# Performance work log

Hardware: AMD Instinct MI355X
Metric: run time of the kernel (lower is better)

The kernel has to match this reference:

```python
import jax, jax.numpy as jnp
import numpy as np

N = 100000      # nodes
E = 3200000     # edges (avg degree 32)
D = 128         # embed_dim
STEP = 1        # number of gnn_conv steps


def setup_inputs() -> dict:
    key = jax.random.key(0)
    k1, k2, k3, k4, k5 = jax.random.split(key, 5)
    hidden = jax.random.normal(k1, (N, D), dtype=jnp.float32)
    src = jax.random.randint(k2, (E,), 0, N)
    dst = jax.random.randint(k3, (E,), 0, N)
    # nn.Linear(D, 3D, bias=False) -> store transposed as [D, 3D] for h @ W
    W_h = jax.random.normal(k4, (D, 3 * D), dtype=jnp.float32) * 0.05
    W_hf = jax.random.normal(k5, (D, 2 * D), dtype=jnp.float32) * 0.05
    return {"hidden": hidden, "src": src, "dst": dst, "W_h": W_h, "W_hf": W_hf}


def _graph_conv(h, src, dst, n):
    # DGL GraphConv(norm='both', weight=False, bias=False):
    # h_dst = d_in(dst)^{-1/2} * sum_{(src->dst)} d_out(src)^{-1/2} * h_src
    ones = jnp.ones(src.shape[0], dtype=h.dtype)
    out_deg = jnp.clip(jax.ops.segment_sum(ones, src, num_segments=n), 1.0)
    in_deg = jnp.clip(jax.ops.segment_sum(ones, dst, num_segments=n), 1.0)
    h_norm = h * jax.lax.rsqrt(out_deg)[:, None]          # [N, D]
    agg = jax.ops.segment_sum(h_norm[src], dst, num_segments=n)  # [N, D]
    return agg * jax.lax.rsqrt(in_deg)[:, None]


def reference(hidden, src, dst, W_h, W_hf):
    n = hidden.shape[0]
    seqs = []
    for _ in range(STEP):
        h1, h2, h3 = jnp.split(hidden @ W_h, 3, axis=-1)   # each [N, D]
        conv = _graph_conv(h1, src, dst, n)                 # sparse aggregation
        f1, f2 = jnp.split(conv @ W_hf, 2, axis=-1)         # each [N, D]
        gate = jax.nn.relu(f1 + h2)
        hidden = h3 + gate * f2
        seqs.append(hidden)
    return hidden, jnp.stack(seqs, axis=1).mean(axis=1)
```

## Files before the change

kernel.cpp:

```cpp
#include <hip/hip_runtime.h>

#define N_NODES 100000
#define N_EDGES 3200000
#define DIM 128

#define NB 391
#define GCAP 9216
#define PCHUNK 4096

typedef __attribute__((ext_vector_type(8))) short bf16x8;
typedef __attribute__((ext_vector_type(4))) float f32x4;

__device__ __forceinline__ unsigned short f2bf(float x) {
    unsigned u = __float_as_uint(x);
    unsigned r = (u + 0x7FFF + ((u >> 16) & 1)) >> 16;
    return (unsigned short)r;
}

__device__ __forceinline__ void gld_lds16(const unsigned short* src, unsigned short* dst) {
    __builtin_amdgcn_global_load_lds(
        (const __attribute__((address_space(1))) unsigned int*)src,
        (__attribute__((address_space(3))) unsigned int*)dst, 16, 0, 0);
}

__global__ __launch_bounds__(256) void partition_kernel(const int* __restrict__ src,
                                                        const int* __restrict__ dst,
                                                        int* __restrict__ gcnt_d,
                                                        int* __restrict__ gcnt_s,
                                                        unsigned* __restrict__ bstore_d,
                                                        unsigned* __restrict__ bstore_s) {
    __shared__ int hist_d[NB], hofs_d[NB], cur_d[NB];
    __shared__ int hist_s[NB], hofs_s[NB], cur_s[NB];
    int t = threadIdx.x;
    for (int b = t; b < NB; b += 256) {
        hist_d[b] = 0; cur_d[b] = 0;
        hist_s[b] = 0; cur_s[b] = 0;
    }
    __syncthreads();
    int e0 = blockIdx.x * PCHUNK;
    int n = min(PCHUNK, N_EDGES - e0);
    for (int i = t; i < n; i += 256) {
        int s = src[e0 + i];
        int d = dst[e0 + i];
        atomicAdd(&hist_d[d >> 8], 1);
        atomicAdd(&hist_s[s >> 8], 1);
    }
    __syncthreads();
    for (int b = t; b < NB; b += 256) {
        hofs_d[b] = (hist_d[b] > 0) ? atomicAdd(&gcnt_d[b], hist_d[b]) : 0;
        hofs_s[b] = (hist_s[b] > 0) ? atomicAdd(&gcnt_s[b], hist_s[b]) : 0;
    }
    __syncthreads();
    for (int i = t; i < n; i += 256) {
        int s = src[e0 + i];
        int d = dst[e0 + i];
        int bd = d >> 8;
        int pd = hofs_d[bd] + atomicAdd(&cur_d[bd], 1);
        if (pd < GCAP)
            bstore_d[(size_t)bd * GCAP + pd] = ((unsigned)(d & 255) << 24) | (unsigned)s;
        int bs = s >> 8;
        int ps = hofs_s[bs] + atomicAdd(&cur_s[bs], 1);
        if (ps < GCAP)
            bstore_s[(size_t)bs * GCAP + ps] = (unsigned)(s & 255);
    }
}

__global__ void scanb_kernel(const int* __restrict__ gcnt_d, int* __restrict__ bucket_base,
                             int* __restrict__ row_start) {
    __shared__ int v[512];
    int t = threadIdx.x;
    v[t] = (t < NB) ? min(gcnt_d[t], GCAP) : 0;
    __syncthreads();
    for (int off = 1; off < 512; off <<= 1) {
        int x = (t >= off) ? v[t - off] : 0;
        __syncthreads();
        v[t] += x;
        __syncthreads();
    }
    if (t < NB) bucket_base[t + 1] = v[t];
    if (t == 0) {
        bucket_base[0] = 0;
        row_start[N_NODES] = v[NB - 1];
    }
}

__global__ __launch_bounds__(256) void count_kernel(const int* __restrict__ gcnt_s,
                                                    const unsigned* __restrict__ bstore_s,
                                                    float* __restrict__ rn_out) {
    __shared__ int lcnt[256];
    int b = blockIdx.x;
    int t = threadIdx.x;
    lcnt[t] = 0;
    __syncthreads();
    int cnt = min(gcnt_s[b], GCAP);
    const unsigned* bs = &bstore_s[(size_t)b * GCAP];
    for (int i = t; i < cnt; i += 256)
        atomicAdd(&lcnt[bs[i] & 255], 1);
    __syncthreads();
    int node = b * 256 + t;
    if (node < N_NODES)
        rn_out[node] = rsqrtf((float)max(lcnt[t], 1));
}

__global__ __launch_bounds__(256) void fill2_kernel(const int* __restrict__ gcnt_d,
                                                    const unsigned* __restrict__ bstore_d,
                                                    const int* __restrict__ bucket_base,
                                                    int* __restrict__ col,
                                                    int* __restrict__ row_start,
                                                    float* __restrict__ rn_in) {
    __shared__ int lcnt[256];
    __shared__ int lpre[256];
    __shared__ int lcur[256];
    __shared__ int stage[GCAP];
    int b = blockIdx.x;
    int t = threadIdx.x;
    int node0 = b * 256;
    int nn = min(256, N_NODES - node0);
    lcnt[t] = 0;
    __syncthreads();
    int cnt = min(gcnt_d[b], GCAP);
    int base = bucket_base[b];
    const unsigned* bs = &bstore_d[(size_t)b * GCAP];
    for (int i = t; i < cnt; i += 256)
        atomicAdd(&lcnt[bs[i] >> 24], 1);
    __syncthreads();
    int myc = lcnt[t];
    lpre[t] = myc;
    __syncthreads();
    for (int off = 1; off < 256; off <<= 1) {
        int x = (t >= off) ? lpre[t - off] : 0;
        __syncthreads();
        lpre[t] += x;
        __syncthreads();
    }
    int excl = lpre[t] - myc;
    if (t < nn) {
        row_start[node0 + t] = base + excl;
        rn_in[node0 + t] = rsqrtf((float)max(myc, 1));
    }
    lcur[t] = excl;
    __syncthreads();
    for (int i = t; i < cnt; i += 256) {
        unsigned e = bs[i];
        int p = atomicAdd(&lcur[e >> 24], 1);
        stage[p] = (int)(e & 0xFFFFFF);
    }
    __syncthreads();
    for (int i = t; i < cnt; i += 256)
        col[base + i] = stage[i];
}

__global__ void packw_kernel(const float* __restrict__ W_h, const float* __restrict__ W_hf,
                             unsigned short* __restrict__ W1_t,
                             unsigned short* __restrict__ W23_t,
                             unsigned short* __restrict__ Wf_t) {
    int idx = blockIdx.x * 256 + threadIdx.x;
    if (idx < 16384) {
        int n = idx >> 7, k = idx & 127;
        W1_t[idx] = f2bf(W_h[k * 384 + n]);
    } else if (idx < 49152) {
        int j = idx - 16384;
        int n = j >> 7, k = j & 127;
        W23_t[j] = f2bf(W_h[k * 384 + 128 + n]);
    } else if (idx < 81920) {
        int j = idx - 49152;
        int n = j >> 7, k = j & 127;
        Wf_t[j] = f2bf(W_hf[k * 256 + n]);
    }
}

__global__ __launch_bounds__(256) void packh_kernel(const float* __restrict__ hidden,
                                                    unsigned short* __restrict__ hidden_bf) {
    int i = (blockIdx.x * 256 + threadIdx.x) * 8;
    float4 a = *reinterpret_cast<const float4*>(&hidden[i]);
    float4 b = *reinterpret_cast<const float4*>(&hidden[i + 4]);
    ushort4 lo, hi;
    lo.x = f2bf(a.x); lo.y = f2bf(a.y); lo.z = f2bf(a.z); lo.w = f2bf(a.w);
    hi.x = f2bf(b.x); hi.y = f2bf(b.y); hi.z = f2bf(b.z); hi.w = f2bf(b.w);
    *reinterpret_cast<ushort4*>(&hidden_bf[i]) = lo;
    *reinterpret_cast<ushort4*>(&hidden_bf[i + 4]) = hi;
}

__global__ __launch_bounds__(256) void gemm1_mfma(const unsigned short* __restrict__ hidden_bf,
                                                  const unsigned short* __restrict__ W1_t,
                                                  const float* __restrict__ rn_out,
                                                  unsigned short* __restrict__ h1n) {
    __shared__ __align__(16) unsigned short Bs[16384];
    int t = threadIdx.x;
    int row0 = blockIdx.x * 64;
    int lane = t & 63;
    int wave = t >> 6;
    int wr0 = wave * 16;
    int m = lane & 15;
    int q = lane >> 4;

    int arow = min(row0 + wr0 + m, N_NODES - 1);
    bf16x8 af[4];
#pragma unroll
    for (int kc = 0; kc < 4; ++kc)
        af[kc] = *reinterpret_cast<const bf16x8*>(&hidden_bf[arow * 128 + kc * 32 + q * 8]);
    float s4[4];
#pragma unroll
    for (int reg = 0; reg < 4; ++reg) {
        int row = row0 + wr0 + q * 4 + reg;
        s4[reg] = (row < N_NODES) ? rn_out[row] : 0.f;
    }

#pragma unroll
    for (int i = 0; i < 8; ++i) {
        int G = i * 256 + t;
        int row = G >> 4;
        int kseg = G & 15;
        gld_lds16(&W1_t[row * 128 + ((kseg ^ (row & 7)) * 8)], &Bs[G * 8]);
    }
    __syncthreads();

    f32x4 accn[8];
#pragma unroll
    for (int nt = 0; nt < 8; ++nt) {
        f32x4 acc = {0.f, 0.f, 0.f, 0.f};
#pragma unroll
        for (int kc = 0; kc < 4; ++kc) {
            int g = (nt * 16 + m) * 16 + ((kc * 4 + q) ^ (m & 7));
            bf16x8 b = *reinterpret_cast<const bf16x8*>(&Bs[g * 8]);
            acc = __builtin_amdgcn_mfma_f32_16x16x32_bf16(af[kc], b, acc, 0, 0, 0);
        }
        accn[nt] = acc;
    }
    __syncthreads();

    unsigned short (*Sg)[136] = reinterpret_cast<unsigned short (*)[136]>(&Bs[0]);
#pragma unroll
    for (int nt = 0; nt < 8; ++nt)
#pragma unroll
        for (int reg = 0; reg < 4; ++reg)
            Sg[wr0 + q * 4 + reg][nt * 16 + m] = f2bf(accn[nt][reg] * s4[reg]);
    __syncthreads();
    int seg = (t & 15) * 8;
    int rb = t >> 4;
#pragma unroll
    for (int i = 0; i < 4; ++i) {
        int r = rb + i * 16;
        int row = row0 + r;
        if (row < N_NODES)
            *reinterpret_cast<int4*>(&h1n[row * 128 + seg]) =
                *reinterpret_cast<const int4*>(&Sg[r][seg]);
    }
}

__global__ __launch_bounds__(256) void aggregate_kernel(const unsigned* __restrict__ h1n,
                                                        const int* __restrict__ row_start,
                                                        const int* __restrict__ col,
                                                        const float* __restrict__ rn_in,
                                                        unsigned* __restrict__ conv_bf) {
    int wave = threadIdx.x >> 6;
    int lane = threadIdx.x & 63;
    int node = blockIdx.x * 4 + wave;
    if (node >= N_NODES) return;
    int start = row_start[node];
    int end = row_start[node + 1];
    float ax0 = 0.f, ax1 = 0.f, ay0 = 0.f, ay1 = 0.f;
    for (int j = start; j < end; j += 64) {
        int cnt = min(64, end - j);
        int myc = (lane < cnt) ? col[j + lane] : 0;
        int i = 0;
        for (; i + 16 <= cnt; i += 16) {
            unsigned u[16];
#pragma unroll
            for (int k = 0; k < 16; ++k) {
                int s = __builtin_amdgcn_readlane(myc, i + k);
                u[k] = h1n[s * 64 + lane];
            }
#pragma unroll
            for (int k = 0; k < 16; k += 2) {
                ax0 += __uint_as_float(u[k] << 16);
                ay0 += __uint_as_float(u[k] & 0xFFFF0000u);
                ax1 += __uint_as_float(u[k + 1] << 16);
                ay1 += __uint_as_float(u[k + 1] & 0xFFFF0000u);
            }
        }
        for (; i + 4 <= cnt; i += 4) {
            unsigned u[4];
#pragma unroll
            for (int k = 0; k < 4; ++k) {
                int s = __builtin_amdgcn_readlane(myc, i + k);
                u[k] = h1n[s * 64 + lane];
            }
#pragma unroll
            for (int k = 0; k < 4; k += 2) {
                ax0 += __uint_as_float(u[k] << 16);
                ay0 += __uint_as_float(u[k] & 0xFFFF0000u);
                ax1 += __uint_as_float(u[k + 1] << 16);
                ay1 += __uint_as_float(u[k + 1] & 0xFFFF0000u);
            }
        }
        for (; i < cnt; ++i) {
            int s = __builtin_amdgcn_readlane(myc, i);
            unsigned u = h1n[s * 64 + lane];
            ax0 += __uint_as_float(u << 16);
            ay0 += __uint_as_float(u & 0xFFFF0000u);
        }
    }
    float rn = rn_in[node];
    float ax = ax0 + ax1, ay = ay0 + ay1;
    unsigned packed = ((unsigned)f2bf(ay * rn) << 16) | (unsigned)f2bf(ax * rn);
    conv_bf[node * 64 + lane] = packed;
}

__global__ __launch_bounds__(256) void final_mfma(const unsigned short* __restrict__ hidden_bf,
                                                  const unsigned short* __restrict__ conv_bf,
                                                  const unsigned short* __restrict__ W23_t,
                                                  const unsigned short* __restrict__ Wf_t,
                                                  float* __restrict__ out) {
    __shared__ __align__(16) unsigned short Bst[2][8192];
    int t = threadIdx.x;
    int row0 = blockIdx.x * 64;
    int lane = t & 63;
    int wave = t >> 6;
    int wr0 = wave * 16;
    int m = lane & 15;
    int q = lane >> 4;

    int arow = min(row0 + wr0 + m, N_NODES - 1);
    bf16x8 ah[4], ac[4];
#pragma unroll
    for (int kc = 0; kc < 4; ++kc) {
        int o = arow * 128 + kc * 32 + q * 8;
        ah[kc] = *reinterpret_cast<const bf16x8*>(&hidden_bf[o]);
        ac[kc] = *reinterpret_cast<const bf16x8*>(&conv_bf[o]);
    }

    auto stage = [&](int nt, int buf) {
#pragma unroll
        for (int i = 0; i < 4; ++i) {
            int rowin = t >> 4;
            int kseg = t & 15;
            int srow = ((i & 1) ? (nt + 8) : nt) * 16 + rowin;
            const unsigned short* Wp = (i < 2) ? W23_t : Wf_t;
            gld_lds16(&Wp[srow * 128 + ((kseg ^ (rowin & 7)) * 8)],
                      &Bst[buf][(i * 256 + t) * 8]);
        }
    };

    stage(0, 0);
    __syncthreads();

#pragma unroll
    for (int nt = 0; nt < 8; ++nt) {
        if (nt < 7) stage(nt + 1, (nt + 1) & 1);
        const unsigned short* Bb = Bst[nt & 1];
        f32x4 h2 = {0.f, 0.f, 0.f, 0.f}, h3 = {0.f, 0.f, 0.f, 0.f};
        f32x4 f1 = {0.f, 0.f, 0.f, 0.f}, f2 = {0.f, 0.f, 0.f, 0.f};
#pragma unroll
        for (int kc = 0; kc < 4; ++kc) {
            int ks = (kc * 4 + q) ^ (m & 7);
            bf16x8 b2  = *reinterpret_cast<const bf16x8*>(&Bb[(0 * 256 + m * 16 + ks) * 8]);
            bf16x8 b3  = *reinterpret_cast<const bf16x8*>(&Bb[(1 * 256 + m * 16 + ks) * 8]);
            bf16x8 bf1 = *reinterpret_cast<const bf16x8*>(&Bb[(2 * 256 + m * 16 + ks) * 8]);
            bf16x8 bf2 = *reinterpret_cast<const bf16x8*>(&Bb[(3 * 256 + m * 16 + ks) * 8]);
            h2 = __builtin_amdgcn_mfma_f32_16x16x32_bf16(ah[kc], b2, h2, 0, 0, 0);
            h3 = __builtin_amdgcn_mfma_f32_16x16x32_bf16(ah[kc], b3, h3, 0, 0, 0);
            f1 = __builtin_amdgcn_mfma_f32_16x16x32_bf16(ac[kc], bf1, f1, 0, 0, 0);
            f2 = __builtin_amdgcn_mfma_f32_16x16x32_bf16(ac[kc], bf2, f2, 0, 0, 0);
        }
        int colb = nt * 16 + m;
#pragma unroll
        for (int reg = 0; reg < 4; ++reg) {
            int row = row0 + wr0 + q * 4 + reg;
            float g = fmaxf(f1[reg] + h2[reg], 0.f);
            float o = h3[reg] + g * f2[reg];
            if (row < N_NODES) {
                out[(size_t)row * 128 + colb] = o;
                out[(size_t)(N_NODES + row) * 128 + colb] = o;
            }
        }
        __syncthreads();
    }
}

extern "C" void kernel_launch(void* const* d_in, const int* in_sizes, int n_in,
                              void* d_out, int out_size, void* d_ws, size_t ws_size,
                              hipStream_t stream) {
    const float* hidden = (const float*)d_in[0];
    const int* src = (const int*)d_in[1];
    const int* dst = (const int*)d_in[2];
    const float* W_h = (const float*)d_in[3];
    const float* W_hf = (const float*)d_in[4];
    float* out = (float*)d_out;

    auto align_up = [](size_t x) { return (x + 255) & ~(size_t)255; };
    char* p = (char*)d_ws;
    size_t off = 0;
    unsigned short* h1n = (unsigned short*)(p + off); off += align_up((size_t)N_NODES * 128 * 2);
    unsigned short* conv_bf = (unsigned short*)(p + off); off += align_up((size_t)N_NODES * 128 * 2);
    unsigned short* hidden_bf = (unsigned short*)(p + off); off += align_up((size_t)N_NODES * 128 * 2);
    int* col = (int*)(p + off); off += align_up((size_t)N_EDGES * 4);
    unsigned* bstore_d = (unsigned*)(p + off); off += align_up((size_t)NB * GCAP * 4);
    unsigned* bstore_s = (unsigned*)(p + off); off += align_up((size_t)NB * GCAP * 4);
    int* gcnt_d = (int*)(p + off); off += align_up((size_t)NB * 4);
    int* gcnt_s = (int*)(p + off); off += align_up((size_t)NB * 4);
    int* bucket_base = (int*)(p + off); off += align_up((size_t)(NB + 1) * 4);
    int* row_start = (int*)(p + off); off += align_up((size_t)(N_NODES + 1) * 4);
    float* rn_out = (float*)(p + off); off += align_up((size_t)N_NODES * 4);
    float* rn_in = (float*)(p + off); off += align_up((size_t)N_NODES * 4);
    unsigned short* W1_t = (unsigned short*)(p + off); off += align_up((size_t)128 * 128 * 2);
    unsigned short* W23_t = (unsigned short*)(p + off); off += align_up((size_t)256 * 128 * 2);
    unsigned short* Wf_t = (unsigned short*)(p + off); off += align_up((size_t)256 * 128 * 2);

    (void)hipMemsetAsync(gcnt_d, 0, (size_t)NB * 4, stream);
    (void)hipMemsetAsync(gcnt_s, 0, (size_t)NB * 4, stream);

    partition_kernel<<<(N_EDGES + PCHUNK - 1) / PCHUNK, 256, 0, stream>>>(
        src, dst, gcnt_d, gcnt_s, bstore_d, bstore_s);
    scanb_kernel<<<1, 512, 0, stream>>>(gcnt_d, bucket_base, row_start);
    count_kernel<<<NB, 256, 0, stream>>>(gcnt_s, bstore_s, rn_out);
    fill2_kernel<<<NB, 256, 0, stream>>>(gcnt_d, bstore_d, bucket_base, col, row_start, rn_in);
    packw_kernel<<<(81920 + 255) / 256, 256, 0, stream>>>(W_h, W_hf, W1_t, W23_t, Wf_t);
    packh_kernel<<<(N_NODES * 128) / (256 * 8), 256, 0, stream>>>(hidden, hidden_bf);
    gemm1_mfma<<<(N_NODES + 63) / 64, 256, 0, stream>>>(hidden_bf, W1_t, rn_out, h1n);
    aggregate_kernel<<<(N_NODES + 3) / 4, 256, 0, stream>>>(
        (const unsigned*)h1n, row_start, col, rn_in, (unsigned*)conv_bf);
    final_mfma<<<(N_NODES + 63) / 64, 256, 0, stream>>>(hidden_bf, conv_bf, W23_t, Wf_t, out);
}
```

Baseline: 451.8 us.

## Stage partitioned edges in LDS by bucket before writing, shrink src bucket store to bytes

```diff
diff --git a/kernel.cpp b/kernel.cpp
--- a/kernel.cpp
+++ b/kernel.cpp
@@ -28,14 +28,16 @@
                                                         int* __restrict__ gcnt_d,
                                                         int* __restrict__ gcnt_s,
                                                         unsigned* __restrict__ bstore_d,
-                                                        unsigned* __restrict__ bstore_s) {
-    __shared__ int hist_d[NB], hofs_d[NB], cur_d[NB];
-    __shared__ int hist_s[NB], hofs_s[NB], cur_s[NB];
-    int t = threadIdx.x;
-    for (int b = t; b < NB; b += 256) {
-        hist_d[b] = 0; cur_d[b] = 0;
-        hist_s[b] = 0; cur_s[b] = 0;
-    }
+                                                        unsigned char* __restrict__ bstore_s) {
+    __shared__ int hist_d[NB], cur_d[NB], hofs_d[NB];
+    __shared__ int hist_s[NB], cur_s[NB], hofs_s[NB];
+    __shared__ int vsc_d[512], vsc_s[512];
+    __shared__ unsigned stage_d[PCHUNK];
+    __shared__ unsigned short bmap_d[PCHUNK];
+    __shared__ unsigned char stage_s[PCHUNK];
+    __shared__ unsigned short bmap_s[PCHUNK];
+    int t = threadIdx.x;
+    for (int b = t; b < NB; b += 256) { hist_d[b] = 0; hist_s[b] = 0; }
     __syncthreads();
     int e0 = blockIdx.x * PCHUNK;
     int n = min(PCHUNK, N_EDGES - e0);
@@ -50,18 +52,48 @@
         hofs_d[b] = (hist_d[b] > 0) ? atomicAdd(&gcnt_d[b], hist_d[b]) : 0;
         hofs_s[b] = (hist_s[b] > 0) ? atomicAdd(&gcnt_s[b], hist_s[b]) : 0;
     }
+    vsc_d[t]       = (t < NB) ? hist_d[t] : 0;
+    vsc_d[t + 256] = (t + 256 < NB) ? hist_d[t + 256] : 0;
+    vsc_s[t]       = (t < NB) ? hist_s[t] : 0;
+    vsc_s[t + 256] = (t + 256 < NB) ? hist_s[t + 256] : 0;
+    __syncthreads();
+    for (int off = 1; off < 512; off <<= 1) {
+        int d0 = (t >= off) ? vsc_d[t - off] : 0;
+        int d1 = vsc_d[t + 256 - off];
+        int s0 = (t >= off) ? vsc_s[t - off] : 0;
+        int s1 = vsc_s[t + 256 - off];
+        __syncthreads();
+        vsc_d[t] += d0; vsc_d[t + 256] += d1;
+        vsc_s[t] += s0; vsc_s[t + 256] += s1;
+        __syncthreads();
+    }
+    for (int b = t; b < NB; b += 256) {
+        cur_d[b] = b ? vsc_d[b - 1] : 0;
+        cur_s[b] = b ? vsc_s[b - 1] : 0;
+    }
     __syncthreads();
     for (int i = t; i < n; i += 256) {
         int s = src[e0 + i];
         int d = dst[e0 + i];
         int bd = d >> 8;
-        int pd = hofs_d[bd] + atomicAdd(&cur_d[bd], 1);
-        if (pd < GCAP)
-            bstore_d[(size_t)bd * GCAP + pd] = ((unsigned)(d & 255) << 24) | (unsigned)s;
+        int p = atomicAdd(&cur_d[bd], 1);
+        stage_d[p] = ((unsigned)(d & 255) << 24) | (unsigned)s;
+        bmap_d[p] = (unsigned short)bd;
         int bs = s >> 8;
-        int ps = hofs_s[bs] + atomicAdd(&cur_s[bs], 1);
-        if (ps < GCAP)
-            bstore_s[(size_t)bs * GCAP + ps] = (unsigned)(s & 255);
+        int ps = atomicAdd(&cur_s[bs], 1);
+        stage_s[ps] = (unsigned char)(s & 255);
+        bmap_s[ps] = (unsigned short)bs;
+    }
+    __syncthreads();
+    for (int i = t; i < n; i += 256) {
+        int bd = bmap_d[i];
+        int excl = bd ? vsc_d[bd - 1] : 0;
+        int gp = hofs_d[bd] + (i - excl);
+        if (gp < GCAP) bstore_d[(size_t)bd * GCAP + gp] = stage_d[i];
+        int bs2 = bmap_s[i];
+        int excl2 = bs2 ? vsc_s[bs2 - 1] : 0;
+        int gp2 = hofs_s[bs2] + (i - excl2);
+        if (gp2 < GCAP) bstore_s[(size_t)bs2 * GCAP + gp2] = stage_s[i];
     }
 }
 
@@ -85,7 +117,7 @@
 }
 
 __global__ __launch_bounds__(256) void count_kernel(const int* __restrict__ gcnt_s,
-                                                    const unsigned* __restrict__ bstore_s,
+                                                    const unsigned char* __restrict__ bstore_s,
                                                     float* __restrict__ rn_out) {
     __shared__ int lcnt[256];
     int b = blockIdx.x;
@@ -93,9 +125,9 @@
     lcnt[t] = 0;
     __syncthreads();
     int cnt = min(gcnt_s[b], GCAP);
-    const unsigned* bs = &bstore_s[(size_t)b * GCAP];
+    const unsigned char* bs = &bstore_s[(size_t)b * GCAP];
     for (int i = t; i < cnt; i += 256)
-        atomicAdd(&lcnt[bs[i] & 255], 1);
+        atomicAdd(&lcnt[bs[i]], 1);
     __syncthreads();
     int node = b * 256 + t;
     if (node < N_NODES)
@@ -396,7 +428,7 @@
     unsigned short* hidden_bf = (unsigned short*)(p + off); off += align_up((size_t)N_NODES * 128 * 2);
     int* col = (int*)(p + off); off += align_up((size_t)N_EDGES * 4);
     unsigned* bstore_d = (unsigned*)(p + off); off += align_up((size_t)NB * GCAP * 4);
-    unsigned* bstore_s = (unsigned*)(p + off); off += align_up((size_t)NB * GCAP * 4);
+    unsigned char* bstore_s = (unsigned char*)(p + off); off += align_up((size_t)NB * GCAP);
     int* gcnt_d = (int*)(p + off); off += align_up((size_t)NB * 4);
     int* gcnt_s = (int*)(p + off); off += align_up((size_t)NB * 4);
     int* bucket_base = (int*)(p + off); off += align_up((size_t)(NB + 1) * 4);
```

After: 419.0 us. 7.3% less time.
